# Kernel tuning notes

Measured on AMD Instinct MI355X. Metric: run time of the kernel, lower is better.

Reference implementation:

```python
import jax, jax.numpy as jnp
import numpy as np

B, T, D, H = 2, 2048, 1024, 16
DH = D // H
EPS = 1e-5


def layer_norm(x, g, b):
    m = jnp.mean(x, axis=-1, keepdims=True)
    v = jnp.mean((x - m) ** 2, axis=-1, keepdims=True)
    return (x - m) * jax.lax.rsqrt(v + EPS) * g + b


def setup_inputs() -> dict:
    key = jax.random.key(0)
    ks = jax.random.split(key, 12)
    s = 0.02
    return {
        "x_refined": jax.random.normal(ks[0], (B, T, D), jnp.float32),
        "x_mem": jax.random.normal(ks[1], (B, T, D), jnp.float32),
        "ln_q_g": jnp.ones((D,), jnp.float32), "ln_q_b": jnp.zeros((D,), jnp.float32),
        "ln_kv_g": jnp.ones((D,), jnp.float32), "ln_kv_b": jnp.zeros((D,), jnp.float32),
        "Wq": jax.random.normal(ks[2], (D, D), jnp.float32) * s,
        "bq": jnp.zeros((D,), jnp.float32),
        "Wk": jax.random.normal(ks[3], (D, D), jnp.float32) * s,
        "bk": jnp.zeros((D,), jnp.float32),
        "Wv": jax.random.normal(ks[4], (D, D), jnp.float32) * s,
        "bv": jnp.zeros((D,), jnp.float32),
        "Wo": jax.random.normal(ks[5], (D, D), jnp.float32) * s,
        "bo": jnp.zeros((D,), jnp.float32),
        "ln_f_g": jnp.ones((D,), jnp.float32), "ln_f_b": jnp.zeros((D,), jnp.float32),
        "W1": jax.random.normal(ks[6], (D, 4 * D), jnp.float32) * s,
        "b1": jnp.zeros((4 * D,), jnp.float32),
        "W2": jax.random.normal(ks[7], (4 * D, D), jnp.float32) * s,
        "b2": jnp.zeros((D,), jnp.float32),
        "band": 24,
    }


def reference(x_refined, x_mem, ln_q_g, ln_q_b, ln_kv_g, ln_kv_b,
              Wq, bq, Wk, bk, Wv, bv, Wo, bo,
              ln_f_g, ln_f_b, W1, b1, W2, b2, band):
    Q = layer_norm(x_refined, ln_q_g, ln_q_b)   # (B,T,D)
    KV = layer_norm(x_mem, ln_kv_g, ln_kv_b)    # (B,T,D)

    # projections, split into heads: (B,H,T,DH)
    q = (Q @ Wq + bq).reshape(B, T, H, DH).transpose(0, 2, 1, 3)
    k = (KV @ Wk + bk).reshape(B, T, H, DH).transpose(0, 2, 1, 3)
    v = (KV @ Wv + bv).reshape(B, T, H, DH).transpose(0, 2, 1, 3)

    scores = jnp.einsum('bhtd,bhsd->bhts', q, k) / jnp.sqrt(jnp.float32(DH))
    # banded additive mask: |t - s| <= band allowed (same math as the Python loop)
    idx = jnp.arange(T)
    allowed = jnp.abs(idx[:, None] - idx[None, :]) <= band  # (T,T)
    scores = jnp.where(allowed[None, None], scores, -jnp.inf)
    attn = jax.nn.softmax(scores, axis=-1)

    ctx = jnp.einsum('bhts,bhsd->bhtd', attn, v)            # (B,H,T,DH)
    ctx = ctx.transpose(0, 2, 1, 3).reshape(B, T, D)
    y = x_refined + (ctx @ Wo + bo)

    h = layer_norm(y, ln_f_g, ln_f_b)
    h = jax.nn.gelu(h @ W1 + b1, approximate=False) @ W2 + b2
    return y + h
```

## Files before the change

kernel.cpp:

```cpp
#include <hip/hip_runtime.h>
#include <math.h>
#include <stdint.h>

#define TSEQ   2048
#define DMODEL 1024
#define NHEAD  16
#define DHEAD  64
#define MROWS  4096

typedef short bf16x8 __attribute__((ext_vector_type(8)));
typedef float f32x4  __attribute__((ext_vector_type(4)));
typedef uint64_t u64x2 __attribute__((ext_vector_type(2)));
typedef unsigned short u16;

typedef __attribute__((address_space(3))) unsigned int lds_u32_t;
typedef __attribute__((address_space(1))) unsigned int glb_u32_t;

static __device__ __forceinline__ u16 f2bf(float f) {
    unsigned u = __float_as_uint(f);
    u += 0x7FFFu + ((u >> 16) & 1u);
    return (u16)(u >> 16);
}
static __device__ __forceinline__ float bf2f(u16 h) {
    return __uint_as_float(((unsigned)h) << 16);
}

__global__ __launch_bounds__(256) void tc_kernel(
    const float* __restrict__ W, u16* __restrict__ Wt, int K, int N)
{
    __shared__ u16 tile[32][33];
    const int n0 = blockIdx.x * 32, k0 = blockIdx.y * 32;
    const int t = threadIdx.x;
    const int tx = t & 31, ty = t >> 5;
#pragma unroll
    for (int i = 0; i < 4; ++i) {
        int kk = ty + i * 8;
        tile[kk][tx] = f2bf(W[(size_t)(k0 + kk) * N + n0 + tx]);
    }
    __syncthreads();
#pragma unroll
    for (int i = 0; i < 4; ++i) {
        int nn = ty + i * 8;
        Wt[(size_t)(n0 + nn) * K + k0 + tx] = tile[tx][nn];
    }
}

__global__ __launch_bounds__(256) void biaspack_kernel(
    const float* __restrict__ bq, const float* __restrict__ bk,
    const float* __restrict__ bv, float* __restrict__ o)
{
    const int i = blockIdx.x * 256 + threadIdx.x;
    if (i < 1024) o[i] = bq[i];
    else if (i < 2048) o[i] = bk[i - 1024];
    else if (i < 3072) o[i] = bv[i - 2048];
}

__global__ __launch_bounds__(256) void vt_kernel(
    const u16* __restrict__ qkv, u16* __restrict__ vT)
{
    __shared__ __align__(16) u16 tile[64][72];
    const int bb = blockIdx.z;
    const int t0 = blockIdx.x * 64;
    const int c0 = blockIdx.y * 64;
    const int tid = threadIdx.x;
    const int r = tid >> 2;
    const int c = (tid & 3) * 16;
    const u16* src = qkv + (size_t)(bb * TSEQ + t0 + r) * 3072 + 2048 + c0 + c;
    *(bf16x8*)&tile[r][c]     = *(const bf16x8*)(src);
    *(bf16x8*)&tile[r][c + 8] = *(const bf16x8*)(src + 8);
    __syncthreads();
    u16 o[16];
#pragma unroll
    for (int j = 0; j < 16; ++j) o[j] = tile[c + j][r];
    u16* dst = vT + (size_t)(bb * 1024 + c0 + r) * TSEQ + t0 + c;
    *(bf16x8*)dst       = *(bf16x8*)&o[0];
    *(bf16x8*)(dst + 8) = *(bf16x8*)&o[8];
}

__global__ __launch_bounds__(256) void ln_kernel(
    const float* __restrict__ x, const float* __restrict__ g,
    const float* __restrict__ b, u16* __restrict__ out)
{
    const int row = blockIdx.x;
    const int t = threadIdx.x;
    const float4 v = ((const float4*)(x + (size_t)row * DMODEL))[t];
    float s  = v.x + v.y + v.z + v.w;
    float s2 = v.x * v.x + v.y * v.y + v.z * v.z + v.w * v.w;
#pragma unroll
    for (int m = 32; m >= 1; m >>= 1) { s += __shfl_xor(s, m); s2 += __shfl_xor(s2, m); }
    __shared__ float ps[4], ps2[4];
    if ((t & 63) == 0) { ps[t >> 6] = s; ps2[t >> 6] = s2; }
    __syncthreads();
    const float S  = ps[0] + ps[1] + ps[2] + ps[3];
    const float S2 = ps2[0] + ps2[1] + ps2[2] + ps2[3];
    const float mean = S * (1.0f / DMODEL);
    const float var  = S2 * (1.0f / DMODEL) - mean * mean;
    const float rstd = rsqrtf(var + 1e-5f);
    const float4 gg = ((const float4*)g)[t];
    const float4 bb = ((const float4*)b)[t];
    u16 o[4];
    o[0] = f2bf((v.x - mean) * rstd * gg.x + bb.x);
    o[1] = f2bf((v.y - mean) * rstd * gg.y + bb.y);
    o[2] = f2bf((v.z - mean) * rstd * gg.z + bb.z);
    o[3] = f2bf((v.w - mean) * rstd * gg.w + bb.w);
    *(short4*)(out + (size_t)row * DMODEL + t * 4) = *(short4*)o;
}

template <int EPI>
__global__ __launch_bounds__(256) void gemm_bt(
    const u16* __restrict__ A, const u16* __restrict__ A2,
    const u16* __restrict__ Wt,
    const float* __restrict__ bias, const float* __restrict__ resid,
    u16* __restrict__ Cb, float* __restrict__ Cf, float* __restrict__ Cf2,
    int N, int K, int kl, int gx, int cx)
{
    extern __shared__ __align__(16) char smem[];

    const int bid = blockIdx.x;
    const int xcd = bid & 7, jj = bid >> 3;
    const int sx = gx / cx;
    const int sy = (gridDim.x >> 3) / sx;
    const int xr = xcd / cx, xc = xcd % cx;
    const int jr = jj / sx, jc = jj % sx;
    const int m0 = (xr * sy + jr) * 128;
    const int n0 = (xc * sx + jc) * 128;
    const int kofs = blockIdx.y * kl;

    const int t = threadIdx.x;
    const int lane = t & 63;
    const int wv = t >> 6;
    const int wr = wv >> 1, wc = wv & 1;

    const u16* Ause = (A2 != nullptr && n0 >= 1024) ? A2 : A;

    const int strow = t >> 2;
    const int stcol = (t & 3) * 8;
    const u16* gA  = Ause + (size_t)(m0 + strow) * K + kofs + stcol;
    const u16* gA2 = gA + (size_t)64 * K;
    const u16* gB  = Wt + (size_t)(n0 + strow) * K + kofs + stcol;
    const u16* gB2 = gB + (size_t)64 * K;

#define STAGE(bufi, k0) do {                                                            \
    char* _b = smem + (bufi) * 16384 + wv * 1024;                                       \
    __builtin_amdgcn_global_load_lds((const glb_u32_t*)(gA  + (k0)), (lds_u32_t*)(_b),          16, 0, 0); \
    __builtin_amdgcn_global_load_lds((const glb_u32_t*)(gA2 + (k0)), (lds_u32_t*)(_b + 4096),  16, 0, 0); \
    __builtin_amdgcn_global_load_lds((const glb_u32_t*)(gB  + (k0)), (lds_u32_t*)(_b + 8192),  16, 0, 0); \
    __builtin_amdgcn_global_load_lds((const glb_u32_t*)(gB2 + (k0)), (lds_u32_t*)(_b + 12288), 16, 0, 0); \
} while (0)

    f32x4 zero = {0.f, 0.f, 0.f, 0.f};
    f32x4 acc[4][4];
#pragma unroll
    for (int mi = 0; mi < 4; ++mi)
#pragma unroll
        for (int ni = 0; ni < 4; ++ni) acc[mi][ni] = zero;

    const int fr = lane & 15, fq = lane >> 4;
    const int nk = kl >> 5;

    STAGE(0, 0);
    STAGE(1, 32);

    for (int kt = 0; kt < nk; ++kt) {
        const int cur = kt & 1;
        if (kt < nk - 1) { asm volatile("s_waitcnt vmcnt(4)" ::: "memory"); }
        else             { asm volatile("s_waitcnt vmcnt(0)" ::: "memory"); }
        __builtin_amdgcn_s_barrier();

        const u16* As_ = (const u16*)smem + cur * 8192;
        const u16* Bs_ = As_ + 4096;
        bf16x8 af[4], bfr[4];
#pragma unroll
        for (int mi = 0; mi < 4; ++mi)
            af[mi] = *(const bf16x8*)&As_[(wr * 64 + mi * 16 + fr) * 32 + fq * 8];
#pragma unroll
        for (int ni = 0; ni < 4; ++ni)
            bfr[ni] = *(const bf16x8*)&Bs_[(wc * 64 + ni * 16 + fr) * 32 + fq * 8];

        __builtin_amdgcn_s_setprio(1);
#pragma unroll
        for (int mi = 0; mi < 4; ++mi)
#pragma unroll
            for (int ni = 0; ni < 4; ++ni)
                acc[mi][ni] = __builtin_amdgcn_mfma_f32_16x16x32_bf16(af[mi], bfr[ni], acc[mi][ni], 0, 0, 0);
        __builtin_amdgcn_s_setprio(0);
        __builtin_amdgcn_sched_barrier(0);
        __builtin_amdgcn_s_barrier();
        if (kt + 2 < nk) STAGE(cur, (kt + 2) << 5);
    }
#undef STAGE

    if (EPI <= 1) {
        u16* cs = (u16*)smem;
#pragma unroll
        for (int ni = 0; ni < 4; ++ni) {
            const int col = wc * 64 + ni * 16 + fr;
            const float bv = bias[n0 + col];
#pragma unroll
            for (int mi = 0; mi < 4; ++mi) {
#pragma unroll
                for (int j = 0; j < 4; ++j) {
                    const int row = wr * 64 + mi * 16 + fq * 4 + j;
                    float val = acc[mi][ni][j] + bv;
                    if (EPI == 1)
                        val = 0.5f * val * (1.0f + erff(val * 0.70710678118654752f));
                    cs[row * 132 + col] = f2bf(val);
                }
            }
        }
        __syncthreads();
        const int rr = t >> 4, cc = (t & 15) * 8;
#pragma unroll
        for (int c8 = 0; c8 < 8; ++c8) {
            const int row = c8 * 16 + rr;
            const uint64_t lo = *(const uint64_t*)&cs[row * 132 + cc];
            const uint64_t hi = *(const uint64_t*)&cs[row * 132 + cc + 4];
            u64x2 v; v.x = lo; v.y = hi;
            *(u64x2*)&Cb[(size_t)(m0 + row) * N + n0 + cc] = v;
        }
    } else {
        float* Cpart = (EPI == 3) ? (blockIdx.y ? Cf2 : Cf) : Cf;
#pragma unroll
        for (int ni = 0; ni < 4; ++ni) {
            const int col = n0 + wc * 64 + ni * 16 + fr;
            const float bv = (EPI == 3) ? 0.f : bias[col];
#pragma unroll
            for (int mi = 0; mi < 4; ++mi) {
#pragma unroll
                for (int j = 0; j < 4; ++j) {
                    const int row = m0 + wr * 64 + mi * 16 + fq * 4 + j;
                    float val = acc[mi][ni][j] + bv;
                    if (EPI == 2)
                        Cf[(size_t)row * N + col] = val + resid[(size_t)row * N + col];
                    else
                        Cpart[(size_t)row * N + col] = val;
                }
            }
        }
    }
}

__global__ __launch_bounds__(256) void redk_kernel(
    const float* __restrict__ p0, const float* __restrict__ p1,
    const float* __restrict__ bias, const float* __restrict__ resid,
    float* __restrict__ out, int n4, int ncols)
{
    const int stride = gridDim.x * 256;
    for (int i = blockIdx.x * 256 + threadIdx.x; i < n4; i += stride) {
        const float4 a = ((const float4*)p0)[i];
        const float4 b = ((const float4*)p1)[i];
        const float4 r = ((const float4*)resid)[i];
        const float4 bb = *(const float4*)&bias[(i * 4) & (ncols - 1)];
        float4 o;
        o.x = a.x + b.x + bb.x + r.x;
        o.y = a.y + b.y + bb.y + r.y;
        o.z = a.z + b.z + bb.z + r.z;
        o.w = a.w + b.w + bb.w + r.w;
        ((float4*)out)[i] = o;
    }
}

__global__ __launch_bounds__(256) void battn_kernel(
    const u16* __restrict__ qkv, const u16* __restrict__ vT,
    u16* __restrict__ ctx, const int* __restrict__ band_ptr)
{
    __shared__ __align__(16) u16 P[4][16][104];
    const int band = *band_ptr;
    const int bid = blockIdx.x;
    const int tile = bid & 31;
    const int h = (bid >> 5) & 15;
    const int b = bid >> 9;
    const int w = threadIdx.x >> 6;
    const int lane = threadIdx.x & 63;
    const int fr = lane & 15, fq = lane >> 4;
    const int t0 = tile * 64 + w * 16;

    const size_t qbase = ((size_t)b * TSEQ) * 3072 + h * DHEAD;
    const size_t kbase = qbase + 1024;
    const size_t cbase = ((size_t)b * TSEQ) * DMODEL + h * DHEAD;

    const bf16x8 aq0 = *(const bf16x8*)&qkv[qbase + (size_t)(t0 + fr) * 3072 + fq * 8];
    const bf16x8 aq1 = *(const bf16x8*)&qkv[qbase + (size_t)(t0 + fr) * 3072 + 32 + fq * 8];

    const int kb0 = t0 - 32;
    const f32x4 zero = {0.f, 0.f, 0.f, 0.f};

    f32x4 sc[5];
#pragma unroll
    for (int kt = 0; kt < 5; ++kt) {
        const int srow = kb0 + kt * 16 + fr;
        const int scl = min(max(srow, 0), TSEQ - 1);
        const bf16x8 kf0 = *(const bf16x8*)&qkv[kbase + (size_t)scl * 3072 + fq * 8];
        const bf16x8 kf1 = *(const bf16x8*)&qkv[kbase + (size_t)scl * 3072 + 32 + fq * 8];
        f32x4 a = zero;
        a = __builtin_amdgcn_mfma_f32_16x16x32_bf16(aq0, kf0, a, 0, 0, 0);
        a = __builtin_amdgcn_mfma_f32_16x16x32_bf16(aq1, kf1, a, 0, 0, 0);
        sc[kt] = a;
    }

    float mx[4], l[4];
#pragma unroll
    for (int j = 0; j < 4; ++j) mx[j] = -1e30f;
#pragma unroll
    for (int kt = 0; kt < 5; ++kt) {
        const int s = kb0 + kt * 16 + fr;
#pragma unroll
        for (int j = 0; j < 4; ++j) {
            const int tq = t0 + fq * 4 + j;
            const bool ok = (s >= 0) && (s < TSEQ) && (abs(tq - s) <= band);
            const float vv = ok ? sc[kt][j] * 0.125f : -1e30f;
            sc[kt][j] = vv;
            mx[j] = fmaxf(mx[j], vv);
        }
    }
#pragma unroll
    for (int m = 1; m <= 8; m <<= 1)
#pragma unroll
        for (int j = 0; j < 4; ++j) mx[j] = fmaxf(mx[j], __shfl_xor(mx[j], m));

#pragma unroll
    for (int j = 0; j < 4; ++j) l[j] = 0.f;
#pragma unroll
    for (int kt = 0; kt < 5; ++kt)
#pragma unroll
        for (int j = 0; j < 4; ++j) {
            const float p = __expf(sc[kt][j] - mx[j]);
            sc[kt][j] = p;
            l[j] += p;
        }
#pragma unroll
    for (int m = 1; m <= 8; m <<= 1)
#pragma unroll
        for (int j = 0; j < 4; ++j) l[j] += __shfl_xor(l[j], m);

#pragma unroll
    for (int kt = 0; kt < 5; ++kt)
#pragma unroll
        for (int j = 0; j < 4; ++j)
            P[w][fq * 4 + j][kt * 16 + fr] = f2bf(sc[kt][j]);
    {
        const short4 z4 = {0, 0, 0, 0};
        *(short4*)&P[w][fr][80 + fq * 4] = z4;
    }
    __syncthreads();

    bf16x8 pa[3];
#pragma unroll
    for (int c = 0; c < 3; ++c)
        pa[c] = *(const bf16x8*)&P[w][fr][c * 32 + fq * 8];

    const size_t vbase = ((size_t)(b * NHEAD + h) * DHEAD) * TSEQ;
    f32x4 cacc[4];
#pragma unroll
    for (int dt = 0; dt < 4; ++dt) cacc[dt] = zero;
#pragma unroll
    for (int dt = 0; dt < 4; ++dt) {
#pragma unroll
        for (int c = 0; c < 3; ++c) {
            const int s8 = kb0 + c * 32 + fq * 8;
            const int s8c = min(max(s8, 0), TSEQ - 8);
            const bf16x8 vf = *(const bf16x8*)&vT[vbase + (size_t)(dt * 16 + fr) * TSEQ + s8c];
            cacc[dt] = __builtin_amdgcn_mfma_f32_16x16x32_bf16(pa[c], vf, cacc[dt], 0, 0, 0);
        }
    }

    float rl[4];
#pragma unroll
    for (int j = 0; j < 4; ++j) rl[j] = 1.0f / l[j];
#pragma unroll
    for (int dt = 0; dt < 4; ++dt)
#pragma unroll
        for (int j = 0; j < 4; ++j)
            ctx[cbase + (size_t)(t0 + fq * 4 + j) * DMODEL + dt * 16 + fr] =
                f2bf(cacc[dt][j] * rl[j]);
}

extern "C" void kernel_launch(void* const* d_in, const int* in_sizes, int n_in,
                              void* d_out, int out_size, void* d_ws, size_t ws_size,
                              hipStream_t stream) {
    const float* x_ref  = (const float*)d_in[0];
    const float* x_mem  = (const float*)d_in[1];
    const float* ln_q_g = (const float*)d_in[2];
    const float* ln_q_b = (const float*)d_in[3];
    const float* ln_kv_g= (const float*)d_in[4];
    const float* ln_kv_b= (const float*)d_in[5];
    const float* Wq = (const float*)d_in[6];
    const float* bq = (const float*)d_in[7];
    const float* Wk = (const float*)d_in[8];
    const float* bk = (const float*)d_in[9];
    const float* Wv = (const float*)d_in[10];
    const float* bv = (const float*)d_in[11];
    const float* Wo = (const float*)d_in[12];
    const float* bo = (const float*)d_in[13];
    const float* ln_f_g = (const float*)d_in[14];
    const float* ln_f_b = (const float*)d_in[15];
    const float* W1 = (const float*)d_in[16];
    const float* b1 = (const float*)d_in[17];
    const float* W2 = (const float*)d_in[18];
    const float* b2 = (const float*)d_in[19];
    const int*  band = (const int*)d_in[20];
    float* out = (float*)d_out;

    char* ws = (char*)d_ws;
    const size_t MB = 1024 * 1024;
    if (ws_size < 128 * MB) return;
    u16*   wt_qkv = (u16*)(ws + 0 * MB);
    u16*   wt_o   = (u16*)(ws + 6 * MB);
    u16*   wt_1   = (u16*)(ws + 8 * MB);
    u16*   wt_2   = (u16*)(ws + 16 * MB);
    float* bqkv   = (float*)(ws + 24 * MB);
    u16*   aq     = (u16*)(ws + 25 * MB);
    u16*   akv    = (u16*)(ws + 33 * MB);
    u16*   qkvb   = (u16*)(ws + 41 * MB);
    u16*   vTb    = (u16*)(ws + 65 * MB);
    u16*   ctxb   = (u16*)(ws + 73 * MB);
    float* y      = (float*)(ws + 81 * MB);
    u16*   hb     = (u16*)(ws + 97 * MB);
    u16*   a1     = (u16*)(ws + 25 * MB);
    float* p0     = (float*)(ws + 57 * MB);
    float* p1     = (float*)(ws + 97 * MB);

    dim3 blk(256);
    const size_t SM_GEMM = 32768;
    const size_t SM_BF16 = 33792;

    tc_kernel<<<dim3(32, 32),  blk, 0, stream>>>(Wq, wt_qkv,               1024, 1024);
    tc_kernel<<<dim3(32, 32),  blk, 0, stream>>>(Wk, wt_qkv + 1024 * 1024, 1024, 1024);
    tc_kernel<<<dim3(32, 32),  blk, 0, stream>>>(Wv, wt_qkv + 2048 * 1024, 1024, 1024);
    tc_kernel<<<dim3(32, 32),  blk, 0, stream>>>(Wo, wt_o, 1024, 1024);
    tc_kernel<<<dim3(128, 32), blk, 0, stream>>>(W1, wt_1, 1024, 4096);
    tc_kernel<<<dim3(32, 128), blk, 0, stream>>>(W2, wt_2, 4096, 1024);
    biaspack_kernel<<<12, blk, 0, stream>>>(bq, bk, bv, bqkv);
    ln_kernel<<<MROWS, blk, 0, stream>>>(x_ref, ln_q_g, ln_q_b, aq);
    ln_kernel<<<MROWS, blk, 0, stream>>>(x_mem, ln_kv_g, ln_kv_b, akv);
    gemm_bt<0><<<dim3(768), blk, SM_BF16, stream>>>(aq, akv, wt_qkv, bqkv, nullptr,
                                                    qkvb, nullptr, nullptr,
                                                    3072, 1024, 1024, 24, 2);
    vt_kernel<<<dim3(32, 16, 2), blk, 0, stream>>>(qkvb, vTb);
    battn_kernel<<<1024, blk, 0, stream>>>(qkvb, vTb, ctxb, band);
    gemm_bt<2><<<dim3(256), blk, SM_GEMM, stream>>>(ctxb, nullptr, wt_o, bo, x_ref,
                                                    nullptr, y, nullptr,
                                                    1024, 1024, 1024, 8, 1);
    ln_kernel<<<MROWS, blk, 0, stream>>>(y, ln_f_g, ln_f_b, hb);
    gemm_bt<1><<<dim3(1024), blk, SM_BF16, stream>>>(hb, nullptr, wt_1, b1, nullptr,
                                                     a1, nullptr, nullptr,
                                                     4096, 1024, 1024, 32, 2);
    gemm_bt<3><<<dim3(256, 2), blk, SM_GEMM, stream>>>(a1, nullptr, wt_2, nullptr, nullptr,
                                                       nullptr, p0, p1,
                                                       1024, 4096, 2048, 8, 1);
    redk_kernel<<<2048, blk, 0, stream>>>(p0, p1, b2, y, out, MROWS * 1024 / 4, 1024);
}
```

Before: 365.6 us.

## Use 256x256-tile 8-wave GEMM with 4-slot LDS pipeline for QKV and FFN1

```diff
diff --git a/kernel.cpp b/kernel.cpp
--- a/kernel.cpp
+++ b/kernel.cpp
@@ -107,6 +107,138 @@
 }
 
 template <int EPI>
+__global__ __launch_bounds__(512, 2) void gemm8(
+    const u16* __restrict__ A, const u16* __restrict__ A2,
+    const u16* __restrict__ Wt, const float* __restrict__ bias,
+    u16* __restrict__ Cb, int N, int K, int gx, int cx)
+{
+    __shared__ __align__(16) char smem8[131072];
+
+    const int bid = blockIdx.x;
+    const int xcd = bid & 7, jj = bid >> 3;
+    const int sx = gx / cx;
+    const int sy = (gridDim.x >> 3) / sx;
+    const int xr = xcd / cx, xc = xcd % cx;
+    const int jr = jj / sx, jc = jj % sx;
+    const int m0 = (xr * sy + jr) * 256;
+    const int n0 = (xc * sx + jc) * 256;
+
+    const int tid = threadIdx.x;
+    const int lane = tid & 63;
+    const int w = tid >> 6;
+    const int wr = w >> 2, wc = w & 3;
+    const int fr = lane & 15, fq = lane >> 4;
+    const int swzoff = (fq ^ ((fr >> 1) & 3)) * 16;
+
+    const u16* Ause = (A2 != nullptr && n0 >= 1024) ? A2 : A;
+
+    const int strow = tid >> 2;
+    const int stcol = ((tid & 3) ^ ((tid >> 3) & 3)) * 8;
+    const u16* gAs = Ause + (size_t)(m0 + strow) * K + stcol;
+    const u16* gBs = Wt  + (size_t)(n0 + strow) * K + stcol;
+
+#define STAGE_A(slot, kt) do {                                                           \
+    const u16* _s = gAs + (size_t)(kt) * 32;                                             \
+    char* _l = smem8 + (slot) * 32768 + w * 1024;                                        \
+    __builtin_amdgcn_global_load_lds((const glb_u32_t*)_s, (lds_u32_t*)_l, 16, 0, 0);    \
+    __builtin_amdgcn_global_load_lds((const glb_u32_t*)(_s + (size_t)128 * K),           \
+                                     (lds_u32_t*)(_l + 8192), 16, 0, 0);                 \
+} while (0)
+#define STAGE_B(slot, kt) do {                                                           \
+    const u16* _s = gBs + (size_t)(kt) * 32;                                             \
+    char* _l = smem8 + (slot) * 32768 + 16384 + w * 1024;                                \
+    __builtin_amdgcn_global_load_lds((const glb_u32_t*)_s, (lds_u32_t*)_l, 16, 0, 0);    \
+    __builtin_amdgcn_global_load_lds((const glb_u32_t*)(_s + (size_t)128 * K),           \
+                                     (lds_u32_t*)(_l + 8192), 16, 0, 0);                 \
+} while (0)
+
+    f32x4 zero = {0.f, 0.f, 0.f, 0.f};
+    f32x4 acc[8][4];
+#pragma unroll
+    for (int mi = 0; mi < 8; ++mi)
+#pragma unroll
+        for (int ni = 0; ni < 4; ++ni) acc[mi][ni] = zero;
+
+    const int nt = K >> 5;
+    STAGE_A(0, 0); STAGE_B(0, 0);
+    STAGE_A(1, 1); STAGE_B(1, 1);
+
+    const int abase = (wr * 128 + fr) * 64 + swzoff;
+    const int bbase = 16384 + (wc * 64 + fr) * 64 + swzoff;
+
+    for (int t = 0; t < nt; ++t) {
+        const int slot = t & 3;
+        const char* sb = smem8 + slot * 32768;
+        asm volatile("s_waitcnt vmcnt(4)" ::: "memory");
+        __builtin_amdgcn_s_barrier();
+
+        bf16x8 bfr[4], af[4];
+#pragma unroll
+        for (int ni = 0; ni < 4; ++ni)
+            bfr[ni] = *(const bf16x8*)(sb + bbase + ni * 1024);
+#pragma unroll
+        for (int mi = 0; mi < 4; ++mi)
+            af[mi] = *(const bf16x8*)(sb + abase + mi * 1024);
+        if (t + 2 < nt) STAGE_A((t + 2) & 3, t + 2);
+        __builtin_amdgcn_s_setprio(1);
+#pragma unroll
+        for (int mi = 0; mi < 4; ++mi)
+#pragma unroll
+            for (int ni = 0; ni < 4; ++ni)
+                acc[mi][ni] = __builtin_amdgcn_mfma_f32_16x16x32_bf16(af[mi], bfr[ni], acc[mi][ni], 0, 0, 0);
+        __builtin_amdgcn_s_setprio(0);
+
+        bf16x8 af2[4];
+#pragma unroll
+        for (int mi = 0; mi < 4; ++mi)
+            af2[mi] = *(const bf16x8*)(sb + abase + (mi + 4) * 1024);
+        if (t + 2 < nt) STAGE_B((t + 2) & 3, t + 2);
+        __builtin_amdgcn_s_setprio(1);
+#pragma unroll
+        for (int mi = 0; mi < 4; ++mi)
+#pragma unroll
+            for (int ni = 0; ni < 4; ++ni)
+                acc[mi + 4][ni] = __builtin_amdgcn_mfma_f32_16x16x32_bf16(af2[mi], bfr[ni], acc[mi + 4][ni], 0, 0, 0);
+        __builtin_amdgcn_s_setprio(0);
+    }
+#undef STAGE_A
+#undef STAGE_B
+
+    u16* cs = (u16*)smem8;
+#pragma unroll
+    for (int hh = 0; hh < 2; ++hh) {
+        __builtin_amdgcn_s_barrier();
+        if (wr == hh) {
+#pragma unroll
+            for (int ni = 0; ni < 4; ++ni) {
+                const int col = wc * 64 + ni * 16 + fr;
+                const float bv = bias[n0 + col];
+#pragma unroll
+                for (int mi = 0; mi < 8; ++mi) {
+#pragma unroll
+                    for (int j = 0; j < 4; ++j) {
+                        float val = acc[mi][ni][j] + bv;
+                        if (EPI == 1)
+                            val = 0.5f * val * (1.0f + erff(val * 0.70710678118654752f));
+                        cs[(mi * 16 + fq * 4 + j) * 260 + col] = f2bf(val);
+                    }
+                }
+            }
+        }
+        __builtin_amdgcn_s_barrier();
+        const int cc = (tid & 31) * 8;
+#pragma unroll
+        for (int p = 0; p < 8; ++p) {
+            const int row = p * 16 + (tid >> 5);
+            const uint64_t lo = *(const uint64_t*)&cs[row * 260 + cc];
+            const uint64_t hi = *(const uint64_t*)&cs[row * 260 + cc + 4];
+            u64x2 v; v.x = lo; v.y = hi;
+            *(u64x2*)&Cb[(size_t)(m0 + hh * 128 + row) * N + n0 + cc] = v;
+        }
+    }
+}
+
+template <int EPI>
 __global__ __launch_bounds__(256) void gemm_bt(
     const u16* __restrict__ A, const u16* __restrict__ A2,
     const u16* __restrict__ Wt,
@@ -190,51 +322,21 @@
     }
 #undef STAGE
 
-    if (EPI <= 1) {
-        u16* cs = (u16*)smem;
-#pragma unroll
-        for (int ni = 0; ni < 4; ++ni) {
-            const int col = wc * 64 + ni * 16 + fr;
-            const float bv = bias[n0 + col];
-#pragma unroll
-            for (int mi = 0; mi < 4; ++mi) {
-#pragma unroll
-                for (int j = 0; j < 4; ++j) {
-                    const int row = wr * 64 + mi * 16 + fq * 4 + j;
-                    float val = acc[mi][ni][j] + bv;
-                    if (EPI == 1)
-                        val = 0.5f * val * (1.0f + erff(val * 0.70710678118654752f));
-                    cs[row * 132 + col] = f2bf(val);
-                }
-            }
-        }
-        __syncthreads();
-        const int rr = t >> 4, cc = (t & 15) * 8;
-#pragma unroll
-        for (int c8 = 0; c8 < 8; ++c8) {
-            const int row = c8 * 16 + rr;
-            const uint64_t lo = *(const uint64_t*)&cs[row * 132 + cc];
-            const uint64_t hi = *(const uint64_t*)&cs[row * 132 + cc + 4];
-            u64x2 v; v.x = lo; v.y = hi;
-            *(u64x2*)&Cb[(size_t)(m0 + row) * N + n0 + cc] = v;
-        }
-    } else {
-        float* Cpart = (EPI == 3) ? (blockIdx.y ? Cf2 : Cf) : Cf;
-#pragma unroll
-        for (int ni = 0; ni < 4; ++ni) {
-            const int col = n0 + wc * 64 + ni * 16 + fr;
-            const float bv = (EPI == 3) ? 0.f : bias[col];
-#pragma unroll
-            for (int mi = 0; mi < 4; ++mi) {
-#pragma unroll
-                for (int j = 0; j < 4; ++j) {
-                    const int row = m0 + wr * 64 + mi * 16 + fq * 4 + j;
-                    float val = acc[mi][ni][j] + bv;
-                    if (EPI == 2)
-                        Cf[(size_t)row * N + col] = val + resid[(size_t)row * N + col];
-                    else
-                        Cpart[(size_t)row * N + col] = val;
-                }
+    float* Cpart = (EPI == 3) ? (blockIdx.y ? Cf2 : Cf) : Cf;
+#pragma unroll
+    for (int ni = 0; ni < 4; ++ni) {
+        const int col = n0 + wc * 64 + ni * 16 + fr;
+        const float bv = (EPI == 3) ? 0.f : bias[col];
+#pragma unroll
+        for (int mi = 0; mi < 4; ++mi) {
+#pragma unroll
+            for (int j = 0; j < 4; ++j) {
+                const int row = m0 + wr * 64 + mi * 16 + fq * 4 + j;
+                float val = acc[mi][ni][j] + bv;
+                if (EPI == 2)
+                    Cf[(size_t)row * N + col] = val + resid[(size_t)row * N + col];
+                else
+                    Cpart[(size_t)row * N + col] = val;
             }
         }
     }
@@ -422,7 +524,6 @@
 
     dim3 blk(256);
     const size_t SM_GEMM = 32768;
-    const size_t SM_BF16 = 33792;
 
     tc_kernel<<<dim3(32, 32),  blk, 0, stream>>>(Wq, wt_qkv,               1024, 1024);
     tc_kernel<<<dim3(32, 32),  blk, 0, stream>>>(Wk, wt_qkv + 1024 * 1024, 1024, 1024);
@@ -433,18 +534,16 @@
     biaspack_kernel<<<12, blk, 0, stream>>>(bq, bk, bv, bqkv);
     ln_kernel<<<MROWS, blk, 0, stream>>>(x_ref, ln_q_g, ln_q_b, aq);
     ln_kernel<<<MROWS, blk, 0, stream>>>(x_mem, ln_kv_g, ln_kv_b, akv);
-    gemm_bt<0><<<dim3(768), blk, SM_BF16, stream>>>(aq, akv, wt_qkv, bqkv, nullptr,
-                                                    qkvb, nullptr, nullptr,
-                                                    3072, 1024, 1024, 24, 2);
+    gemm8<0><<<dim3(192), dim3(512), 0, stream>>>(aq, akv, wt_qkv, bqkv, qkvb,
+                                                  3072, 1024, 12, 2);
     vt_kernel<<<dim3(32, 16, 2), blk, 0, stream>>>(qkvb, vTb);
     battn_kernel<<<1024, blk, 0, stream>>>(qkvb, vTb, ctxb, band);
     gemm_bt<2><<<dim3(256), blk, SM_GEMM, stream>>>(ctxb, nullptr, wt_o, bo, x_ref,
                                                     nullptr, y, nullptr,
                                                     1024, 1024, 1024, 8, 1);
     ln_kernel<<<MROWS, blk, 0, stream>>>(y, ln_f_g, ln_f_b, hb);
-    gemm_bt<1><<<dim3(1024), blk, SM_BF16, stream>>>(hb, nullptr, wt_1, b1, nullptr,
-                                                     a1, nullptr, nullptr,
-                                                     4096, 1024, 1024, 32, 2);
+    gemm8<1><<<dim3(256), dim3(512), 0, stream>>>(hb, nullptr, wt_1, b1, a1,
+                                                  4096, 1024, 16, 2);
     gemm_bt<3><<<dim3(256, 2), blk, SM_GEMM, stream>>>(a1, nullptr, wt_2, nullptr, nullptr,
                                                        nullptr, p0, p1,
                                                        1024, 4096, 2048, 8, 1);
```

Measured after the change: 384.8 us. 1.05x slower.
